# Optimization experiments

Hardware: AMD Instinct MI355X
Metric: run time of the kernel (lower is better)

The kernel has to match this reference:

```python
import jax, jax.numpy as jnp
import numpy as np

B, F, S, P, E, H = 64, 32, 512, 96, 8, 2048
TOP_K = 2
ALPHA = 10.0
ENT_EPS = 1e-8
CV_EPS = 1e-10


def setup_inputs() -> dict:
    key = jax.random.key(0)
    ks = jax.random.split(key, 8)
    s = 0.02
    return {
        "x": jax.random.normal(ks[0], (B, F, S), dtype=jnp.float32),
        "time_embedding": jax.random.normal(ks[1], (B, F, S), dtype=jnp.float32),
        "Wg": jax.random.normal(ks[2], (S, E), dtype=jnp.float32) * s,
        "bg": jnp.zeros((E,), dtype=jnp.float32),
        "W1": jax.random.normal(ks[3], (E, S, H), dtype=jnp.float32) * s,
        "b1": jnp.zeros((E, H), dtype=jnp.float32),
        "W2": jax.random.normal(ks[4], (E, H, P), dtype=jnp.float32) * s,
        "b2": jnp.zeros((E, P), dtype=jnp.float32),
    }


def _gates(tf, Wg, bg):
    # tf: [F, B, S] -> logits [F, B, E]
    logits = jnp.einsum('fbs,se->fbe', tf, Wg) + bg
    # kthvalue(x, E - top_k + 1) = (E - top_k)-th entry (0-based) of ascending sort = k-th largest
    kth = jnp.sort(logits, axis=-1)[..., E - TOP_K]  # [F, B]
    mask = logits < kth[..., None]
    sm = jax.nn.softmax(logits, axis=-1)
    dec = jnp.where(mask, ALPHA * jnp.log(sm + 1.0), ALPHA * (jnp.exp(sm) - 1.0))
    return jax.nn.softmax(dec, axis=-1)  # [F, B, E]


def reference(x, time_embedding, Wg, bg, W1, b1, W2, b2):
    xf = jnp.transpose(x, (1, 0, 2))               # [F, B, S]
    tf = jnp.transpose(time_embedding, (1, 0, 2))  # [F, B, S]
    gates = _gates(tf, Wg, bg)                     # [F, B, E]

    # all experts on all features (eval mode: dropout = identity)
    h = jax.nn.gelu(jnp.einsum('fbs,esh->febh', xf, W1) + b1[None, :, None, :], approximate=False)
    eo = jnp.einsum('febh,ehp->febp', h, W2) + b2[None, :, None, :]  # [F, E, B, P]
    out = jnp.einsum('fbe,febp->fbp', gates, eo)   # gated weighted sum
    output = jnp.transpose(out, (1, 0, 2))         # [B, F, P]

    # selector loss: cv_squared of importance = gates.sum(batch) expanded over pred_len
    gsum = gates.sum(axis=1)                       # [F, E]
    imp = jnp.broadcast_to(gsum[..., None], (F, E, P)).reshape(F, E * P)
    cv = jnp.var(imp, axis=1, ddof=1) / (jnp.mean(imp, axis=1) ** 2 + CV_EPS)
    selector_loss = jnp.sum(cv)                    # loss_coef = 1.0

    # entropy loss: importance1 = gates.mean(batch) expanded over pred_len
    gmean = gates.mean(axis=1)                     # [F, E]
    imp1 = jnp.broadcast_to(gmean[..., None], (F, E, P))
    entropy_loss = jnp.sum((-imp1 * jnp.log(imp1 + ENT_EPS)).mean(axis=(1, 2)))

    return output, selector_loss, entropy_loss
```

## Files before the change

kernel.cpp:

```cpp
#include <hip/hip_runtime.h>
#include <math.h>

#define B_ 64
#define F_ 32
#define S_ 512
#define P_ 96
#define E_ 8
#define H_ 2048
#define M_ 2048

#define BM 128
#define BH 128
#define BK 64
#define ZSPLIT 2
#define HPZ (H_ / ZSPLIT)
#define NHT (HPZ / BH)
#define NKC (S_ / BK)

typedef __bf16 bf16x8 __attribute__((ext_vector_type(8)));
typedef __bf16 bf16x4 __attribute__((ext_vector_type(4)));
typedef float f32x4 __attribute__((ext_vector_type(4)));

#define MFMA16(a, b, c) __builtin_amdgcn_mfma_f32_16x16x32_bf16((a), (b), (c), 0, 0, 0)

#define GLL16(gp, lp) __builtin_amdgcn_global_load_lds(                     \
    (const __attribute__((address_space(1))) void*)(gp),                    \
    (__attribute__((address_space(3))) void*)(lp), 16, 0, 0)

__device__ __forceinline__ float fast_gelu(float x) {
  float e = __builtin_amdgcn_exp2f(-2.45546696f * x);
  return x * __builtin_amdgcn_rcpf(1.0f + e);
}

#define PREP_GRID 3776

__global__ __launch_bounds__(256) void k_prep(const float* __restrict__ x,
                                              const float* __restrict__ te,
                                              const float* __restrict__ Wg,
                                              const float* __restrict__ bg,
                                              const float* __restrict__ W1,
                                              const float* __restrict__ W2,
                                              __bf16* __restrict__ xbf,
                                              __bf16* __restrict__ w1t,
                                              __bf16* __restrict__ w2t,
                                              float* __restrict__ gates,
                                              float* __restrict__ out) {
  __shared__ float tile[64 * 65];
  const int blk = blockIdx.x;
  const int tid = threadIdx.x;

  if (blk < 2048) {
    int e = blk >> 8, tt = blk & 255;
    int si = tt >> 5, hi = tt & 31;
    const float* src = W1 + (size_t)e * S_ * H_ + (size_t)(si * 64) * H_ + hi * 64;
    {
      int row = tid >> 2;
      int cb = (tid & 3) * 16;
#pragma unroll
      for (int k = 0; k < 4; ++k) {
        f32x4 v = *(const f32x4*)(src + (size_t)row * H_ + cb + k * 4);
#pragma unroll
        for (int u = 0; u < 4; ++u) tile[row * 65 + cb + k * 4 + u] = v[u];
      }
    }
    __syncthreads();
    {
      int h = tid >> 2;
      int sb = (tid & 3) * 16;
      __bf16* dst = w1t + (size_t)e * H_ * S_ + (size_t)(hi * 64 + h) * S_ + si * 64 + sb;
      bf16x8 o0, o1;
#pragma unroll
      for (int k = 0; k < 8; ++k) o0[k] = (__bf16)tile[(sb + k) * 65 + h];
#pragma unroll
      for (int k = 0; k < 8; ++k) o1[k] = (__bf16)tile[(sb + 8 + k) * 65 + h];
      *(bf16x8*)dst = o0;
      *(bf16x8*)(dst + 8) = o1;
    }
    return;
  }
  if (blk < 2560) {
    int t = blk - 2048;
    int e = t >> 6, hi = (t >> 1) & 31, ph = t & 1;
    const float* src = W2 + (size_t)e * H_ * P_ + (size_t)(hi * 64) * P_ + ph * 48;
    {
      int h = tid & 63;
      int seg = tid >> 6;
#pragma unroll
      for (int k = 0; k < 3; ++k) {
        f32x4 v = *(const f32x4*)(src + (size_t)h * P_ + seg * 12 + k * 4);
#pragma unroll
        for (int u = 0; u < 4; ++u) tile[h * 49 + seg * 12 + k * 4 + u] = v[u];
      }
    }
    __syncthreads();
    if (tid < 192) {
      int p = tid >> 2;
      int hb = (tid & 3) * 16;
      __bf16* dst = w2t + (size_t)e * P_ * H_ + (size_t)(ph * 48 + p) * H_ + hi * 64 + hb;
      bf16x8 o0, o1;
#pragma unroll
      for (int k = 0; k < 8; ++k) o0[k] = (__bf16)tile[(hb + k) * 49 + p];
#pragma unroll
      for (int k = 0; k < 8; ++k) o1[k] = (__bf16)tile[(hb + 8 + k) * 49 + p];
      *(bf16x8*)dst = o0;
      *(bf16x8*)(dst + 8) = o1;
    }
    return;
  }
  if (blk < 3072) {
    size_t i = (size_t)(blk - 2560) * 2048 + (size_t)tid * 8;
#pragma unroll
    for (int k = 0; k < 2; ++k) {
      f32x4 v = *(const f32x4*)(x + i + k * 4);
      bf16x4 o = {(__bf16)v[0], (__bf16)v[1], (__bf16)v[2], (__bf16)v[3]};
      *(bf16x4*)(xbf + i + k * 4) = o;
    }
    return;
  }
  if (blk < 3584) {
    int wave = tid >> 6, lane = tid & 63;
    int m = (blk - 3072) * 4 + wave;
    const float* trow = te + (size_t)m * S_;
    float acc[E_];
#pragma unroll
    for (int e = 0; e < E_; ++e) acc[e] = 0.f;
    for (int s = lane; s < S_; s += 64) {
      float t = trow[s];
      const f32x4* wgr = (const f32x4*)(Wg + s * E_);
      f32x4 a = wgr[0], b = wgr[1];
      acc[0] += t * a[0]; acc[1] += t * a[1]; acc[2] += t * a[2]; acc[3] += t * a[3];
      acc[4] += t * b[0]; acc[5] += t * b[1]; acc[6] += t * b[2]; acc[7] += t * b[3];
    }
#pragma unroll
    for (int e = 0; e < E_; ++e) {
#pragma unroll
      for (int off = 32; off > 0; off >>= 1) acc[e] += __shfl_xor(acc[e], off, 64);
    }
    if (lane == 0) {
      float lg[E_];
      float m1 = -3.4e38f, m2 = -3.4e38f;
#pragma unroll
      for (int e = 0; e < E_; ++e) {
        float v = acc[e] + bg[e];
        lg[e] = v;
        if (v > m1) { m2 = m1; m1 = v; }
        else if (v > m2) { m2 = v; }
      }
      float den = 0.f, sm[E_];
#pragma unroll
      for (int e = 0; e < E_; ++e) { sm[e] = expf(lg[e] - m1); den += sm[e]; }
      float inv = 1.f / den;
      float dmax = -3.4e38f, dec[E_];
#pragma unroll
      for (int e = 0; e < E_; ++e) {
        float p = sm[e] * inv;
        float d = (lg[e] < m2) ? (10.f * logf(p + 1.f)) : (10.f * (expf(p) - 1.f));
        dec[e] = d;
        dmax = fmaxf(dmax, d);
      }
      float dden = 0.f;
#pragma unroll
      for (int e = 0; e < E_; ++e) { dec[e] = expf(dec[e] - dmax); dden += dec[e]; }
      float dinv = 1.f / dden;
#pragma unroll
      for (int e = 0; e < E_; ++e) gates[m * E_ + e] = dec[e] * dinv;
    }
    return;
  }
  {
    size_t i = (size_t)(blk - 3584) * 1024 + (size_t)tid * 4;
    f32x4 z4 = {0.f, 0.f, 0.f, 0.f};
    *(f32x4*)(out + i) = z4;
  }
}

__global__ __launch_bounds__(512, 2) void k_experts(
    const __bf16* __restrict__ xbf,
    const __bf16* __restrict__ w1t,
    const __bf16* __restrict__ w2t,
    const float* __restrict__ b1,
    const float* __restrict__ b2,
    const float* __restrict__ gates,
    float* __restrict__ out)
{
  __shared__ __align__(16) __bf16 W1s[2][BH * BK];
  __shared__ __align__(16) __bf16 Xs[2][BM * BK];
  __shared__ __align__(16) __bf16 W2s[P_ * BH];
  __shared__ __align__(16) __bf16 Hs[BM * BH];

  const int tid = threadIdx.x;

  if (blockIdx.z == ZSPLIT) {
    if (blockIdx.x != 0 || blockIdx.y != 0) return;
    float* gsum = (float*)&W1s[0][0];
    float* cvs  = gsum + F_ * E_;
    float* ents = cvs + F_;
    if (tid < 256) {
      int f = tid >> 3, ee = tid & 7;
      float s = 0.f;
      for (int b = 0; b < B_; ++b) s += gates[(size_t)(b * F_ + f) * E_ + ee];
      gsum[f * E_ + ee] = s;
    }
    __syncthreads();
    if (tid < F_) {
      float mean = 0.f;
#pragma unroll
      for (int k = 0; k < E_; ++k) mean += gsum[tid * E_ + k];
      mean *= (1.f / E_);
      float ss = 0.f;
#pragma unroll
      for (int k = 0; k < E_; ++k) { float d = gsum[tid * E_ + k] - mean; ss += d * d; }
      float var = (float)P_ * ss / (float)(E_ * P_ - 1);
      cvs[tid] = var / (mean * mean + 1e-10f);
      float ent = 0.f;
#pragma unroll
      for (int k = 0; k < E_; ++k) { float g = gsum[tid * E_ + k] * (1.f / B_); ent += -g * logf(g + 1e-8f); }
      ents[tid] = ent * (1.f / E_);
    }
    __syncthreads();
    if (tid == 0) {
      float a = 0.f, b = 0.f;
      for (int k = 0; k < F_; ++k) { a += cvs[k]; b += ents[k]; }
      out[(size_t)M_ * P_ + 0] = a;
      out[(size_t)M_ * P_ + 1] = b;
    }
    return;
  }

  const int wave = tid >> 6, lane = tid & 63;
  const int l15 = lane & 15, quad = lane >> 4;
  const int e = blockIdx.x;
  const int m0 = blockIdx.y * BM;
  const int hz = blockIdx.z * HPZ;

  const int sg = lane & 7;
  const int srl = lane >> 3;
  const int gcol = ((sg ^ srl) * 8);

  const __bf16* w1base = w1t + ((size_t)e * H_ + hz + wave * 16 + srl) * S_ + gcol;
  const __bf16* xg = xbf + (size_t)(m0 + wave * 16 + srl) * S_ + gcol;
  const __bf16* w2z = w2t + (size_t)e * P_ * H_ + hz;

  const int hq = (wave & 1) * 64;
  const int mq = (wave >> 1) * 32;
  const int w16 = wave * 16;

  const f32x4 fz = {0.f, 0.f, 0.f, 0.f};
  f32x4 acc1[4][2];
  f32x4 acc2[6];
#pragma unroll
  for (int j = 0; j < 6; ++j) acc2[j] = fz;

  auto STAGE = [&](int ht_, int kc_, int b) {
    const __bf16* w1p = w1base + (size_t)(ht_ * BH) * S_ + kc_ * BK;
    const __bf16* xp  = xg + kc_ * BK;
#pragma unroll
    for (int p = 0; p < 2; ++p) {
      GLL16(w1p + (size_t)(p * 8) * S_, &W1s[b][(wave * 16 + p * 8) * BK]);
      GLL16(xp  + (size_t)(p * 8) * S_, &Xs[b][(wave * 16 + p * 8) * BK]);
    }
  };

  auto STAGEW2 = [&](int ht_) {
#pragma unroll
    for (int p = 0; p < 3; ++p) {
      int r2 = wave * 12 + p * 4 + quad;
      GLL16(w2z + (size_t)r2 * H_ + ht_ * BH + ((l15 ^ (r2 & 7)) * 8),
            &W2s[(wave * 12 + p * 4) * BH]);
    }
  };

  auto COMPUTE = [&](int b) {
#pragma unroll
    for (int kk = 0; kk < 2; ++kk) {
      bf16x8 af[4], bx[2];
#pragma unroll
      for (int i = 0; i < 4; ++i) {
        int r = hq + i * 16 + l15;
        af[i] = *(const bf16x8*)&W1s[b][r * BK + (((kk * 4 + quad) ^ (r & 7)) * 8)];
      }
#pragma unroll
      for (int j = 0; j < 2; ++j) {
        int r = mq + j * 16 + l15;
        bx[j] = *(const bf16x8*)&Xs[b][r * BK + (((kk * 4 + quad) ^ (r & 7)) * 8)];
      }
#pragma unroll
      for (int i = 0; i < 4; ++i)
#pragma unroll
        for (int j = 0; j < 2; ++j)
          acc1[i][j] = MFMA16(af[i], bx[j], acc1[i][j]);
    }
  };

  auto GEMM2Q = [&](int kk) {
    int ab = (w16 + l15) * 256 + (((kk * 4 + quad) ^ l15) * 16);
    bf16x8 a = *(const bf16x8*)((const char*)Hs + ab);
#pragma unroll
    for (int j = 0; j < 6; ++j) {
      bf16x8 bb = *(const bf16x8*)&W2s[(j * 16 + l15) * BH + (((kk * 4 + quad) ^ (l15 & 7)) * 8)];
      acc2[j] = MFMA16(a, bb, acc2[j]);
    }
  };

  auto GELU = [&](int ht_) {
    const float* b1w = b1 + (size_t)e * H_ + hz + ht_ * BH;
#pragma unroll
    for (int i = 0; i < 4; ++i) {
      int h = hq + i * 16 + quad * 4;
      f32x4 bv = *(const f32x4*)(b1w + h);
#pragma unroll
      for (int j = 0; j < 2; ++j) {
        bf16x4 hv;
#pragma unroll
        for (int r = 0; r < 4; ++r)
          hv[r] = (__bf16)fast_gelu(acc1[i][j][r] + bv[r]);
        int m = mq + j * 16 + l15;
        int wb = m * 256 + (((h >> 3) ^ l15) * 16) + (quad & 1) * 8;
        *(bf16x4*)((char*)Hs + wb) = hv;
      }
    }
  };

  STAGE(0, 0, 0);
  __syncthreads();

  for (int ht = 0; ht < NHT; ++ht) {
#pragma unroll
    for (int i = 0; i < 4; ++i)
#pragma unroll
      for (int j = 0; j < 2; ++j) acc1[i][j] = fz;

    int bsel = 0;
#pragma unroll
    for (int kc = 0; kc < NKC; ++kc) {
      if (kc < NKC - 1) {
        STAGE(ht, kc + 1, bsel ^ 1);
      } else {
        if (ht < NHT - 1) STAGE(ht + 1, 0, bsel ^ 1);
        STAGEW2(ht);
      }
      if (kc < 4 && ht > 0) GEMM2Q(kc);

      COMPUTE(bsel);
      __syncthreads();
      bsel ^= 1;
    }
    GELU(ht);
    __syncthreads();
  }
#pragma unroll
  for (int kk = 0; kk < 4; ++kk) GEMM2Q(kk);

#pragma unroll
  for (int r = 0; r < 4; ++r) {
    int m = m0 + w16 + quad * 4 + r;
    float g = gates[m * E_ + e];
#pragma unroll
    for (int j = 0; j < 6; ++j) {
      int col = j * 16 + l15;
      float v = acc2[j][r];
      if (blockIdx.z == 0) v += b2[e * P_ + col];
      atomicAdd(&out[(size_t)m * P_ + col], g * v);
    }
  }
}

extern "C" void kernel_launch(void* const* d_in, const int* in_sizes, int n_in,
                              void* d_out, int out_size, void* d_ws, size_t ws_size,
                              hipStream_t stream) {
  const float* x  = (const float*)d_in[0];
  const float* te = (const float*)d_in[1];
  const float* Wg = (const float*)d_in[2];
  const float* bg = (const float*)d_in[3];
  const float* W1 = (const float*)d_in[4];
  const float* b1 = (const float*)d_in[5];
  const float* W2 = (const float*)d_in[6];
  const float* b2 = (const float*)d_in[7];
  float* out = (float*)d_out;

  char* ws = (char*)d_ws;
  float* gates = (float*)ws;
  __bf16* xbf  = (__bf16*)(ws + 65536);
  __bf16* w1t  = (__bf16*)(ws + 65536 + 2097152);
  __bf16* w2t  = (__bf16*)(ws + 65536 + 2097152 + 16777216);

  k_prep<<<PREP_GRID, 256, 0, stream>>>(x, te, Wg, bg, W1, W2, xbf, w1t, w2t, gates, out);
  k_experts<<<dim3(E_, M_ / BM, ZSPLIT + 1), 512, 0, stream>>>(xbf, w1t, w2t, b1, b2, gates, out);
}
```

Measured before the change: 185.4 us.

## Load GEMM operands directly from global memory instead of LDS staging

Removes the double-buffered LDS staging of W1, X and W2 tiles, which used async global-to-LDS loads, and has each wave read its MFMA fragments directly from global memory. Only the H tile stays in shared memory, which cuts LDS use and drops the per-k-chunk barriers. The occupancy hint in launch_bounds is removed. The cost is many uncoalesced 16-byte global loads, with reuse across waves now left to the cache. Load latency is also no longer hidden by a staging pipeline.

```diff
diff --git a/kernel.cpp b/kernel.cpp
--- a/kernel.cpp
+++ b/kernel.cpp
@@ -11,21 +11,15 @@
 
 #define BM 128
 #define BH 128
-#define BK 64
 #define ZSPLIT 2
 #define HPZ (H_ / ZSPLIT)
 #define NHT (HPZ / BH)
-#define NKC (S_ / BK)
 
 typedef __bf16 bf16x8 __attribute__((ext_vector_type(8)));
 typedef __bf16 bf16x4 __attribute__((ext_vector_type(4)));
 typedef float f32x4 __attribute__((ext_vector_type(4)));
 
 #define MFMA16(a, b, c) __builtin_amdgcn_mfma_f32_16x16x32_bf16((a), (b), (c), 0, 0, 0)
-
-#define GLL16(gp, lp) __builtin_amdgcn_global_load_lds(                     \
-    (const __attribute__((address_space(1))) void*)(gp),                    \
-    (__attribute__((address_space(3))) void*)(lp), 16, 0, 0)
 
 __device__ __forceinline__ float fast_gelu(float x) {
   float e = __builtin_amdgcn_exp2f(-2.45546696f * x);
@@ -174,7 +168,7 @@
   }
 }
 
-__global__ __launch_bounds__(512, 2) void k_experts(
+__global__ __launch_bounds__(512) void k_experts(
     const __bf16* __restrict__ xbf,
     const __bf16* __restrict__ w1t,
     const __bf16* __restrict__ w2t,
@@ -183,16 +177,13 @@
     const float* __restrict__ gates,
     float* __restrict__ out)
 {
-  __shared__ __align__(16) __bf16 W1s[2][BH * BK];
-  __shared__ __align__(16) __bf16 Xs[2][BM * BK];
-  __shared__ __align__(16) __bf16 W2s[P_ * BH];
   __shared__ __align__(16) __bf16 Hs[BM * BH];
 
   const int tid = threadIdx.x;
 
   if (blockIdx.z == ZSPLIT) {
     if (blockIdx.x != 0 || blockIdx.y != 0) return;
-    float* gsum = (float*)&W1s[0][0];
+    float* gsum = (float*)&Hs[0];
     float* cvs  = gsum + F_ * E_;
     float* ents = cvs + F_;
     if (tid < 256) {
@@ -233,72 +224,53 @@
   const int m0 = blockIdx.y * BM;
   const int hz = blockIdx.z * HPZ;
 
-  const int sg = lane & 7;
-  const int srl = lane >> 3;
-  const int gcol = ((sg ^ srl) * 8);
-
-  const __bf16* w1base = w1t + ((size_t)e * H_ + hz + wave * 16 + srl) * S_ + gcol;
-  const __bf16* xg = xbf + (size_t)(m0 + wave * 16 + srl) * S_ + gcol;
-  const __bf16* w2z = w2t + (size_t)e * P_ * H_ + hz;
-
   const int hq = (wave & 1) * 64;
   const int mq = (wave >> 1) * 32;
   const int w16 = wave * 16;
 
+  const __bf16* w1l = w1t + ((size_t)e * H_ + hz + hq + l15) * S_ + quad * 8;
+  const __bf16* xl  = xbf + (size_t)(m0 + mq + l15) * S_ + quad * 8;
+  const __bf16* w2l = w2t + ((size_t)e * P_ + l15) * H_ + hz + quad * 8;
+
   const f32x4 fz = {0.f, 0.f, 0.f, 0.f};
   f32x4 acc1[4][2];
   f32x4 acc2[6];
 #pragma unroll
   for (int j = 0; j < 6; ++j) acc2[j] = fz;
 
-  auto STAGE = [&](int ht_, int kc_, int b) {
-    const __bf16* w1p = w1base + (size_t)(ht_ * BH) * S_ + kc_ * BK;
-    const __bf16* xp  = xg + kc_ * BK;
-#pragma unroll
-    for (int p = 0; p < 2; ++p) {
-      GLL16(w1p + (size_t)(p * 8) * S_, &W1s[b][(wave * 16 + p * 8) * BK]);
-      GLL16(xp  + (size_t)(p * 8) * S_, &Xs[b][(wave * 16 + p * 8) * BK]);
+  auto GEMM1 = [&](int ht_) {
+    const __bf16* w1c = w1l + (size_t)(ht_ * BH) * S_;
+#pragma unroll
+    for (int kc = 0; kc < 8; ++kc) {
+#pragma unroll
+      for (int kk = 0; kk < 2; ++kk) {
+        const int ko = kc * 64 + kk * 32;
+        bf16x8 af[4], bx[2];
+#pragma unroll
+        for (int i = 0; i < 4; ++i)
+          af[i] = *(const bf16x8*)(w1c + (size_t)(i * 16) * S_ + ko);
+#pragma unroll
+        for (int j = 0; j < 2; ++j)
+          bx[j] = *(const bf16x8*)(xl + (size_t)(j * 16) * S_ + ko);
+#pragma unroll
+        for (int i = 0; i < 4; ++i)
+#pragma unroll
+          for (int j = 0; j < 2; ++j)
+            acc1[i][j] = MFMA16(af[i], bx[j], acc1[i][j]);
+      }
     }
   };
 
-  auto STAGEW2 = [&](int ht_) {
-#pragma unroll
-    for (int p = 0; p < 3; ++p) {
-      int r2 = wave * 12 + p * 4 + quad;
-      GLL16(w2z + (size_t)r2 * H_ + ht_ * BH + ((l15 ^ (r2 & 7)) * 8),
-            &W2s[(wave * 12 + p * 4) * BH]);
-    }
-  };
-
-  auto COMPUTE = [&](int b) {
-#pragma unroll
-    for (int kk = 0; kk < 2; ++kk) {
-      bf16x8 af[4], bx[2];
-#pragma unroll
-      for (int i = 0; i < 4; ++i) {
-        int r = hq + i * 16 + l15;
-        af[i] = *(const bf16x8*)&W1s[b][r * BK + (((kk * 4 + quad) ^ (r & 7)) * 8)];
-      }
-#pragma unroll
-      for (int j = 0; j < 2; ++j) {
-        int r = mq + j * 16 + l15;
-        bx[j] = *(const bf16x8*)&Xs[b][r * BK + (((kk * 4 + quad) ^ (r & 7)) * 8)];
-      }
-#pragma unroll
-      for (int i = 0; i < 4; ++i)
-#pragma unroll
-        for (int j = 0; j < 2; ++j)
-          acc1[i][j] = MFMA16(af[i], bx[j], acc1[i][j]);
-    }
-  };
-
-  auto GEMM2Q = [&](int kk) {
-    int ab = (w16 + l15) * 256 + (((kk * 4 + quad) ^ l15) * 16);
-    bf16x8 a = *(const bf16x8*)((const char*)Hs + ab);
-#pragma unroll
-    for (int j = 0; j < 6; ++j) {
-      bf16x8 bb = *(const bf16x8*)&W2s[(j * 16 + l15) * BH + (((kk * 4 + quad) ^ (l15 & 7)) * 8)];
-      acc2[j] = MFMA16(a, bb, acc2[j]);
+  auto GEMM2 = [&](int htc) {
+#pragma unroll
+    for (int kk = 0; kk < 4; ++kk) {
+      int ab = (w16 + l15) * 256 + (((kk * 4 + quad) ^ l15) * 16);
+      bf16x8 a = *(const bf16x8*)((const char*)Hs + ab);
+#pragma unroll
+      for (int j = 0; j < 6; ++j) {
+        bf16x8 bb = *(const bf16x8*)(w2l + (size_t)(j * 16) * H_ + htc * BH + kk * 32);
+        acc2[j] = MFMA16(a, bb, acc2[j]);
+      }
     }
   };
 
@@ -321,35 +293,19 @@
     }
   };
 
-  STAGE(0, 0, 0);
-  __syncthreads();
-
   for (int ht = 0; ht < NHT; ++ht) {
 #pragma unroll
     for (int i = 0; i < 4; ++i)
 #pragma unroll
       for (int j = 0; j < 2; ++j) acc1[i][j] = fz;
 
-    int bsel = 0;
-#pragma unroll
-    for (int kc = 0; kc < NKC; ++kc) {
-      if (kc < NKC - 1) {
-        STAGE(ht, kc + 1, bsel ^ 1);
-      } else {
-        if (ht < NHT - 1) STAGE(ht + 1, 0, bsel ^ 1);
-        STAGEW2(ht);
-      }
-      if (kc < 4 && ht > 0) GEMM2Q(kc);
-
-      COMPUTE(bsel);
-      __syncthreads();
-      bsel ^= 1;
-    }
+    GEMM1(ht);
+    if (ht > 0) GEMM2(ht - 1);
+    __syncthreads();
     GELU(ht);
     __syncthreads();
   }
-#pragma unroll
-  for (int kk = 0; kk < 4; ++kk) GEMM2Q(kk);
+  GEMM2(NHT - 1);
 
 #pragma unroll
   for (int r = 0; r < 4; ++r) {
```

Result: slower. 314.1 us (+69.4%).

## Double the M tile, split H four ways, read W2 from global

Applied to the files above, without the earlier changes.

Each block now covers 256 tokens instead of 128, so every W1 tile staged in LDS feeds twice as many MFMAs. The H dimension is split four ways instead of two, so the total block count stays the same. The W2 LDS staging buffer and its loads are removed, and the second GEMM reads W2 fragments straight from global memory. In exchange, occupancy drops to one 512-thread block per CU, and W2 reads become strided global loads in the inner loop. The extra Z split also doubles the atomic adds into the output.

```diff
diff --git a/kernel.cpp b/kernel.cpp
--- a/kernel.cpp
+++ b/kernel.cpp
@@ -9,10 +9,10 @@
 #define H_ 2048
 #define M_ 2048
 
-#define BM 128
+#define BM 256
 #define BH 128
 #define BK 64
-#define ZSPLIT 2
+#define ZSPLIT 4
 #define HPZ (H_ / ZSPLIT)
 #define NHT (HPZ / BH)
 #define NKC (S_ / BK)
@@ -174,7 +174,7 @@
   }
 }
 
-__global__ __launch_bounds__(512, 2) void k_experts(
+__global__ __launch_bounds__(512, 1) void k_experts(
     const __bf16* __restrict__ xbf,
     const __bf16* __restrict__ w1t,
     const __bf16* __restrict__ w2t,
@@ -185,14 +185,13 @@
 {
   __shared__ __align__(16) __bf16 W1s[2][BH * BK];
   __shared__ __align__(16) __bf16 Xs[2][BM * BK];
-  __shared__ __align__(16) __bf16 W2s[P_ * BH];
   __shared__ __align__(16) __bf16 Hs[BM * BH];
 
   const int tid = threadIdx.x;
 
   if (blockIdx.z == ZSPLIT) {
     if (blockIdx.x != 0 || blockIdx.y != 0) return;
-    float* gsum = (float*)&W1s[0][0];
+    float* gsum = (float*)&Hs[0];
     float* cvs  = gsum + F_ * E_;
     float* ents = cvs + F_;
     if (tid < 256) {
@@ -238,67 +237,67 @@
   const int gcol = ((sg ^ srl) * 8);
 
   const __bf16* w1base = w1t + ((size_t)e * H_ + hz + wave * 16 + srl) * S_ + gcol;
-  const __bf16* xg = xbf + (size_t)(m0 + wave * 16 + srl) * S_ + gcol;
+  const __bf16* xg = xbf + (size_t)(m0 + wave * 32 + srl) * S_ + gcol;
   const __bf16* w2z = w2t + (size_t)e * P_ * H_ + hz;
 
   const int hq = (wave & 1) * 64;
-  const int mq = (wave >> 1) * 32;
-  const int w16 = wave * 16;
+  const int mq = (wave >> 1) * 64;
+  const int w32 = wave * 32;
 
   const f32x4 fz = {0.f, 0.f, 0.f, 0.f};
-  f32x4 acc1[4][2];
-  f32x4 acc2[6];
-#pragma unroll
-  for (int j = 0; j < 6; ++j) acc2[j] = fz;
+  f32x4 acc1[4][4];
+  f32x4 acc2[2][6];
+#pragma unroll
+  for (int rt = 0; rt < 2; ++rt)
+#pragma unroll
+    for (int j = 0; j < 6; ++j) acc2[rt][j] = fz;
 
   auto STAGE = [&](int ht_, int kc_, int b) {
     const __bf16* w1p = w1base + (size_t)(ht_ * BH) * S_ + kc_ * BK;
     const __bf16* xp  = xg + kc_ * BK;
 #pragma unroll
-    for (int p = 0; p < 2; ++p) {
+    for (int p = 0; p < 2; ++p)
       GLL16(w1p + (size_t)(p * 8) * S_, &W1s[b][(wave * 16 + p * 8) * BK]);
-      GLL16(xp  + (size_t)(p * 8) * S_, &Xs[b][(wave * 16 + p * 8) * BK]);
-    }
+#pragma unroll
+    for (int p = 0; p < 4; ++p)
+      GLL16(xp + (size_t)(p * 8) * S_, &Xs[b][(wave * 32 + p * 8) * BK]);
   };
 
-  auto STAGEW2 = [&](int ht_) {
-#pragma unroll
-    for (int p = 0; p < 3; ++p) {
-      int r2 = wave * 12 + p * 4 + quad;
-      GLL16(w2z + (size_t)r2 * H_ + ht_ * BH + ((l15 ^ (r2 & 7)) * 8),
-            &W2s[(wave * 12 + p * 4) * BH]);
-    }
-  };
-
   auto COMPUTE = [&](int b) {
 #pragma unroll
     for (int kk = 0; kk < 2; ++kk) {
-      bf16x8 af[4], bx[2];
+      bf16x8 af[4], bx[4];
 #pragma unroll
       for (int i = 0; i < 4; ++i) {
         int r = hq + i * 16 + l15;
         af[i] = *(const bf16x8*)&W1s[b][r * BK + (((kk * 4 + quad) ^ (r & 7)) * 8)];
       }
 #pragma unroll
-      for (int j = 0; j < 2; ++j) {
+      for (int j = 0; j < 4; ++j) {
         int r = mq + j * 16 + l15;
         bx[j] = *(const bf16x8*)&Xs[b][r * BK + (((kk * 4 + quad) ^ (r & 7)) * 8)];
       }
 #pragma unroll
       for (int i = 0; i < 4; ++i)
 #pragma unroll
-        for (int j = 0; j < 2; ++j)
+        for (int j = 0; j < 4; ++j)
           acc1[i][j] = MFMA16(af[i], bx[j], acc1[i][j]);
     }
   };
 
-  auto GEMM2Q = [&](int kk) {
-    int ab = (w16 + l15) * 256 + (((kk * 4 + quad) ^ l15) * 16);
-    bf16x8 a = *(const bf16x8*)((const char*)Hs + ab);
+  auto GEMM2Q = [&](int htc, int kk) {
+    bf16x8 a0, a1;
+    {
+      int ab0 = (w32 + l15) * 256 + (((kk * 4 + quad) ^ l15) * 16);
+      int ab1 = (w32 + 16 + l15) * 256 + (((kk * 4 + quad) ^ l15) * 16);
+      a0 = *(const bf16x8*)((const char*)Hs + ab0);
+      a1 = *(const bf16x8*)((const char*)Hs + ab1);
+    }
 #pragma unroll
     for (int j = 0; j < 6; ++j) {
-      bf16x8 bb = *(const bf16x8*)&W2s[(j * 16 + l15) * BH + (((kk * 4 + quad) ^ (l15 & 7)) * 8)];
-      acc2[j] = MFMA16(a, bb, acc2[j]);
+      bf16x8 bb = *(const bf16x8*)(w2z + (size_t)(j * 16 + l15) * H_ + htc * BH + kk * 32 + quad * 8);
+      acc2[0][j] = MFMA16(a0, bb, acc2[0][j]);
+      acc2[1][j] = MFMA16(a1, bb, acc2[1][j]);
     }
   };
 
@@ -309,7 +308,7 @@
       int h = hq + i * 16 + quad * 4;
       f32x4 bv = *(const f32x4*)(b1w + h);
 #pragma unroll
-      for (int j = 0; j < 2; ++j) {
+      for (int j = 0; j < 4; ++j) {
         bf16x4 hv;
 #pragma unroll
         for (int r = 0; r < 4; ++r)
@@ -328,18 +327,17 @@
 #pragma unroll
     for (int i = 0; i < 4; ++i)
 #pragma unroll
-      for (int j = 0; j < 2; ++j) acc1[i][j] = fz;
+      for (int j = 0; j < 4; ++j) acc1[i][j] = fz;
 
     int bsel = 0;
 #pragma unroll
     for (int kc = 0; kc < NKC; ++kc) {
       if (kc < NKC - 1) {
         STAGE(ht, kc + 1, bsel ^ 1);
-      } else {
-        if (ht < NHT - 1) STAGE(ht + 1, 0, bsel ^ 1);
-        STAGEW2(ht);
-      }
-      if (kc < 4 && ht > 0) GEMM2Q(kc);
+      } else if (ht < NHT - 1) {
+        STAGE(ht + 1, 0, bsel ^ 1);
+      }
+      if (kc < 4 && ht > 0) GEMM2Q(ht - 1, kc);
 
       COMPUTE(bsel);
       __syncthreads();
@@ -349,18 +347,21 @@
     __syncthreads();
   }
 #pragma unroll
-  for (int kk = 0; kk < 4; ++kk) GEMM2Q(kk);
-
-#pragma unroll
-  for (int r = 0; r < 4; ++r) {
-    int m = m0 + w16 + quad * 4 + r;
-    float g = gates[m * E_ + e];
-#pragma unroll
-    for (int j = 0; j < 6; ++j) {
-      int col = j * 16 + l15;
-      float v = acc2[j][r];
-      if (blockIdx.z == 0) v += b2[e * P_ + col];
-      atomicAdd(&out[(size_t)m * P_ + col], g * v);
+  for (int kk = 0; kk < 4; ++kk) GEMM2Q(NHT - 1, kk);
+
+#pragma unroll
+  for (int rt = 0; rt < 2; ++rt) {
+#pragma unroll
+    for (int r = 0; r < 4; ++r) {
+      int m = m0 + w32 + rt * 16 + quad * 4 + r;
+      float g = gates[m * E_ + e];
+#pragma unroll
+      for (int j = 0; j < 6; ++j) {
+        int col = j * 16 + l15;
+        float v = acc2[rt][j][r];
+        if (blockIdx.z == 0) v += b2[e * P_ + col];
+        atomicAdd(&out[(size_t)m * P_ + col], g * v);
+      }
     }
   }
 }
```

After: 217.1 us. +17.1%, slower.
